# Optimization experiments

Measured on AMD Instinct MI355X. Metric: run time of the kernel, lower is better.

## Reference

```python
import jax, jax.numpy as jnp
import numpy as np


def setup_inputs() -> dict:
    key = jax.random.key(0)
    k = jax.random.split(key, 5)
    B, D, T = 8, 512, 8192
    Dh = D // 8
    return {
        "x": jax.random.normal(k[0], (B, D, T), dtype=jnp.float32),
        "w1": jax.random.normal(k[1], (Dh, D), dtype=jnp.float32) * (1.0 / np.sqrt(D)),
        "b1": jax.random.normal(k[2], (Dh,), dtype=jnp.float32) * 0.01,
        "w2": jax.random.normal(k[3], (D, Dh), dtype=jnp.float32) * (1.0 / np.sqrt(Dh)),
        "b2": jax.random.normal(k[4], (D,), dtype=jnp.float32) * 0.01,
        "chunksize": 16,
    }


def reference(x, w1, b1, w2, b2, chunksize):
    # x: [B, D, T]
    B, D, T = x.shape
    pad = (T + chunksize - 1) // chunksize * chunksize - T  # static under jit
    Tp = T + pad
    xp = jnp.pad(x, ((0, 0), (0, 0), (0, pad)))
    # causal cumulative average over time
    denom = jnp.arange(1, Tp + 1, dtype=x.dtype)
    avg = jnp.cumsum(xp, axis=2) / denom  # [B, D, Tp]
    pooled = avg[:, :, chunksize - 1::chunksize]  # [B, D, Tc]
    # SE bottleneck (1x1 convs)
    h = jax.nn.relu(jnp.einsum('od,bdt->bot', w1, pooled) + b1[:, None])
    g = jax.nn.sigmoid(jnp.einsum('od,bdt->bot', w2, h) + b2[:, None])  # [B, D, Tc]
    # upsample gate to per-frame resolution and apply to residual
    up = jnp.repeat(g, chunksize, axis=2)[:, :, :T]
    return up * x
```

## Files before the change

### kernel.cpp

```cpp
#include <hip/hip_runtime.h>
#include <math.h>

#define BB 8
#define DD 512
#define DH 64
#define TT 8192
#define CS 16
#define CC 512

__device__ __forceinline__ float sigf(float v) {
    return 1.0f / (1.0f + __expf(-v));
}

__global__ __launch_bounds__(256) void k_pool(
        const float* __restrict__ x, float* __restrict__ pooled) {
    const int row = blockIdx.x;
    const int t = threadIdx.x;
    const float4* xr = (const float4*)(x + (size_t)row * TT);

    __shared__ float psum[2048];
    __shared__ float wtot[4];

    #pragma unroll
    for (int k = 0; k < 8; k++) {
        float4 v = xr[t + k * 256];
        psum[t + k * 256] = (v.x + v.y) + (v.z + v.w);
    }
    __syncthreads();

    const float4* ps4 = (const float4*)psum;
    float4 q0 = ps4[2 * t];
    float4 q1 = ps4[2 * t + 1];
    float c0 = (q0.x + q0.y) + (q0.z + q0.w);
    float c1 = (q1.x + q1.y) + (q1.z + q1.w);

    float ps = c0 + c1;
    float v = ps;
    int lane = t & 63;
    #pragma unroll
    for (int off = 1; off < 64; off <<= 1) {
        float n = __shfl_up(v, off, 64);
        if (lane >= off) v += n;
    }
    int wid = t >> 6;
    if (lane == 63) wtot[wid] = v;
    __syncthreads();
    float wpre = 0.0f;
    for (int w = 0; w < wid; w++) wpre += wtot[w];
    float incl = v + wpre;
    float excl = incl - ps;
    float s0 = excl + c0;
    float s1 = s0 + c1;
    int c = 2 * t;
    float2 outv;
    outv.x = s0 / (float)(CS * (c + 1));
    outv.y = s1 / (float)(CS * (c + 2));
    ((float2*)(pooled + (size_t)row * CC))[t] = outv;
}

#define PSTR 516

__global__ __launch_bounds__(256) void k_fused(
        const float* __restrict__ x,
        const float* __restrict__ pooled,
        const float* __restrict__ w1, const float* __restrict__ b1,
        const float* __restrict__ w2, const float* __restrict__ b2,
        float* __restrict__ out) {
    const int b = blockIdx.y;
    const int c0 = blockIdx.x * 4;
    const int t = threadIdx.x;

    __shared__ float p[4 * PSTR];
    __shared__ float hs[DH * 4];
    __shared__ float gs[DD * 4];

    {
        const float4* src = (const float4*)(pooled + (size_t)b * DD * CC + c0);
        float4 v0 = src[(size_t)t * (CC / 4)];
        float4 v1 = src[((size_t)t + 256) * (CC / 4)];
        p[0 * PSTR + t] = v0.x; p[1 * PSTR + t] = v0.y;
        p[2 * PSTR + t] = v0.z; p[3 * PSTR + t] = v0.w;
        p[0 * PSTR + t + 256] = v1.x; p[1 * PSTR + t + 256] = v1.y;
        p[2 * PSTR + t + 256] = v1.z; p[3 * PSTR + t + 256] = v1.w;
    }
    __syncthreads();

    const int o = t >> 2, c = t & 3;
    const float4* w1r = (const float4*)(w1 + (size_t)o * DD);
    const float4* pc = (const float4*)(p + c * PSTR);
    float a0 = 0.f, a1 = 0.f, a2 = 0.f, a3 = 0.f;
    #pragma unroll 4
    for (int d4 = 0; d4 < 128; d4++) {
        float4 wv = w1r[d4];
        float4 pv = pc[d4];
        a0 = fmaf(wv.x, pv.x, a0);
        a1 = fmaf(wv.y, pv.y, a1);
        a2 = fmaf(wv.z, pv.z, a2);
        a3 = fmaf(wv.w, pv.w, a3);
    }
    float hv = ((a0 + a1) + (a2 + a3)) + b1[o];
    hs[t] = fmaxf(hv, 0.0f);
    __syncthreads();

    {
        const float4* h4 = (const float4*)hs;
        const float4* w2a = (const float4*)(w2 + (size_t)t * DH);
        const float4* w2b = (const float4*)(w2 + ((size_t)t + 256) * DH);
        float gA0 = 0, gA1 = 0, gA2 = 0, gA3 = 0;
        float gB0 = 0, gB1 = 0, gB2 = 0, gB3 = 0;
        #pragma unroll 4
        for (int q = 0; q < 16; q++) {
            float4 wa = w2a[q];
            float4 wb = w2b[q];
            float4 hA = h4[4 * q + 0];
            float4 hB = h4[4 * q + 1];
            float4 hC = h4[4 * q + 2];
            float4 hD = h4[4 * q + 3];
            gA0 = fmaf(wa.x, hA.x, gA0); gA0 = fmaf(wa.y, hB.x, gA0);
            gA0 = fmaf(wa.z, hC.x, gA0); gA0 = fmaf(wa.w, hD.x, gA0);
            gA1 = fmaf(wa.x, hA.y, gA1); gA1 = fmaf(wa.y, hB.y, gA1);
            gA1 = fmaf(wa.z, hC.y, gA1); gA1 = fmaf(wa.w, hD.y, gA1);
            gA2 = fmaf(wa.x, hA.z, gA2); gA2 = fmaf(wa.y, hB.z, gA2);
            gA2 = fmaf(wa.z, hC.z, gA2); gA2 = fmaf(wa.w, hD.z, gA2);
            gA3 = fmaf(wa.x, hA.w, gA3); gA3 = fmaf(wa.y, hB.w, gA3);
            gA3 = fmaf(wa.z, hC.w, gA3); gA3 = fmaf(wa.w, hD.w, gA3);
            gB0 = fmaf(wb.x, hA.x, gB0); gB0 = fmaf(wb.y, hB.x, gB0);
            gB0 = fmaf(wb.z, hC.x, gB0); gB0 = fmaf(wb.w, hD.x, gB0);
            gB1 = fmaf(wb.x, hA.y, gB1); gB1 = fmaf(wb.y, hB.y, gB1);
            gB1 = fmaf(wb.z, hC.y, gB1); gB1 = fmaf(wb.w, hD.y, gB1);
            gB2 = fmaf(wb.x, hA.z, gB2); gB2 = fmaf(wb.y, hB.z, gB2);
            gB2 = fmaf(wb.z, hC.z, gB2); gB2 = fmaf(wb.w, hD.z, gB2);
            gB3 = fmaf(wb.x, hA.w, gB3); gB3 = fmaf(wb.y, hB.w, gB3);
            gB3 = fmaf(wb.z, hC.w, gB3); gB3 = fmaf(wb.w, hD.w, gB3);
        }
        float bbA = b2[t], bbB = b2[t + 256];
        float4 rA, rB;
        rA.x = sigf(gA0 + bbA); rA.y = sigf(gA1 + bbA);
        rA.z = sigf(gA2 + bbA); rA.w = sigf(gA3 + bbA);
        rB.x = sigf(gB0 + bbB); rB.y = sigf(gB1 + bbB);
        rB.z = sigf(gB2 + bbB); rB.w = sigf(gB3 + bbB);
        float4* gs4 = (float4*)gs;
        gs4[t] = rA;
        gs4[t + 256] = rB;
    }
    __syncthreads();

    {
        const size_t base = (size_t)b * DD * (TT / 4) + (size_t)c0 * 4;
        const float4* x4 = (const float4*)x + base;
        float4* o4 = (float4*)out + base;
        #pragma unroll 8
        for (int k = 0; k < 32; k++) {
            int idx = k * 256 + t;
            int d = idx >> 4;
            int t4 = idx & 15;
            size_t a = (size_t)d * (TT / 4) + t4;
            float4 xv = x4[a];
            float gv = gs[d * 4 + (t4 >> 2)];
            float4 r;
            r.x = xv.x * gv; r.y = xv.y * gv;
            r.z = xv.z * gv; r.w = xv.w * gv;
            o4[a] = r;
        }
    }
}

extern "C" void kernel_launch(void* const* d_in, const int* in_sizes, int n_in,
                              void* d_out, int out_size, void* d_ws, size_t ws_size,
                              hipStream_t stream) {
    const float* x  = (const float*)d_in[0];
    const float* w1 = (const float*)d_in[1];
    const float* b1 = (const float*)d_in[2];
    const float* w2 = (const float*)d_in[3];
    const float* b2 = (const float*)d_in[4];
    float* out = (float*)d_out;

    float* pooled = (float*)d_ws;

    k_pool<<<dim3(BB * DD), dim3(256), 0, stream>>>(x, pooled);
    k_fused<<<dim3(CC / 4, BB), dim3(256), 0, stream>>>(
        x, pooled, w1, b1, w2, b2, out);
}
```

Baseline: 289.0 us.

## Split fused SE gemm and gating into separate kernels with gate buffer

Splits the fused kernel, which ran the SE bottleneck and then applied the gate to strided x tiles, into two kernels. A gemm kernel writes the gate tensor to workspace, and a separate streaming kernel multiplies x by the gate with fully contiguous float4 accesses. The aim is to replace the poorly coalesced 64-byte-per-row accesses of the fused path with linear streaming, and to let the memory-bound pass use all CUs. In exchange it adds a kernel launch and an 8 MB gate write and read round trip.

```diff
diff --git a/kernel.cpp b/kernel.cpp
--- a/kernel.cpp
+++ b/kernel.cpp
@@ -60,19 +60,17 @@
 
 #define PSTR 516
 
-__global__ __launch_bounds__(256) void k_fused(
-        const float* __restrict__ x,
+__global__ __launch_bounds__(256) void k_segemm(
         const float* __restrict__ pooled,
         const float* __restrict__ w1, const float* __restrict__ b1,
         const float* __restrict__ w2, const float* __restrict__ b2,
-        float* __restrict__ out) {
+        float* __restrict__ g) {
     const int b = blockIdx.y;
     const int c0 = blockIdx.x * 4;
     const int t = threadIdx.x;
 
     __shared__ float p[4 * PSTR];
     __shared__ float hs[DH * 4];
-    __shared__ float gs[DD * 4];
 
     {
         const float4* src = (const float4*)(pooled + (size_t)b * DD * CC + c0);
@@ -139,30 +137,44 @@
         rA.z = sigf(gA2 + bbA); rA.w = sigf(gA3 + bbA);
         rB.x = sigf(gB0 + bbB); rB.y = sigf(gB1 + bbB);
         rB.z = sigf(gB2 + bbB); rB.w = sigf(gB3 + bbB);
-        float4* gs4 = (float4*)gs;
-        gs4[t] = rA;
-        gs4[t + 256] = rB;
+        float4* gp = (float4*)(g + (size_t)b * DD * CC + c0);
+        gp[(size_t)t * (CC / 4)] = rA;
+        gp[((size_t)t + 256) * (CC / 4)] = rB;
     }
-    __syncthreads();
+}
 
-    {
-        const size_t base = (size_t)b * DD * (TT / 4) + (size_t)c0 * 4;
-        const float4* x4 = (const float4*)x + base;
-        float4* o4 = (float4*)out + base;
-        #pragma unroll 8
-        for (int k = 0; k < 32; k++) {
-            int idx = k * 256 + t;
-            int d = idx >> 4;
-            int t4 = idx & 15;
-            size_t a = (size_t)d * (TT / 4) + t4;
-            float4 xv = x4[a];
-            float gv = gs[d * 4 + (t4 >> 2)];
-            float4 r;
-            r.x = xv.x * gv; r.y = xv.y * gv;
-            r.z = xv.z * gv; r.w = xv.w * gv;
-            o4[a] = r;
-        }
-    }
+__global__ __launch_bounds__(256) void k_gate(
+        const float* __restrict__ x, const float* __restrict__ g,
+        float* __restrict__ out) {
+    const size_t base = (size_t)blockIdx.x * 1024 + threadIdx.x;
+    const float4* x4 = (const float4*)x;
+    float4* o4 = (float4*)out;
+
+    size_t idx0 = base;
+    size_t idx1 = base + 256;
+    size_t idx2 = base + 512;
+    size_t idx3 = base + 768;
+
+    float4 xv0 = x4[idx0];
+    float4 xv1 = x4[idx1];
+    float4 xv2 = x4[idx2];
+    float4 xv3 = x4[idx3];
+
+    float gv0 = g[(idx0 >> 11) * CC + (int)((idx0 & (TT / 4 - 1)) >> 2)];
+    float gv1 = g[(idx1 >> 11) * CC + (int)((idx1 & (TT / 4 - 1)) >> 2)];
+    float gv2 = g[(idx2 >> 11) * CC + (int)((idx2 & (TT / 4 - 1)) >> 2)];
+    float gv3 = g[(idx3 >> 11) * CC + (int)((idx3 & (TT / 4 - 1)) >> 2)];
+
+    float4 r0, r1, r2, r3;
+    r0.x = xv0.x * gv0; r0.y = xv0.y * gv0; r0.z = xv0.z * gv0; r0.w = xv0.w * gv0;
+    r1.x = xv1.x * gv1; r1.y = xv1.y * gv1; r1.z = xv1.z * gv1; r1.w = xv1.w * gv1;
+    r2.x = xv2.x * gv2; r2.y = xv2.y * gv2; r2.z = xv2.z * gv2; r2.w = xv2.w * gv2;
+    r3.x = xv3.x * gv3; r3.y = xv3.y * gv3; r3.z = xv3.z * gv3; r3.w = xv3.w * gv3;
+
+    o4[idx0] = r0;
+    o4[idx1] = r1;
+    o4[idx2] = r2;
+    o4[idx3] = r3;
 }
 
 extern "C" void kernel_launch(void* const* d_in, const int* in_sizes, int n_in,
@@ -176,8 +188,9 @@
     float* out = (float*)d_out;
 
     float* pooled = (float*)d_ws;
+    float* g      = (float*)((char*)d_ws + (size_t)BB * DD * CC * 4);
 
     k_pool<<<dim3(BB * DD), dim3(256), 0, stream>>>(x, pooled);
-    k_fused<<<dim3(CC / 4, BB), dim3(256), 0, stream>>>(
-        x, pooled, w1, b1, w2, b2, out);
+    k_segemm<<<dim3(CC / 4, BB), dim3(256), 0, stream>>>(pooled, w1, b1, w2, b2, g);
+    k_gate<<<dim3(BB * DD * TT / 4 / 1024), dim3(256), 0, stream>>>(x, g, out);
 }
```

Result: slower. 302.0 us (+4.5%).
